# Performance work log

Measured on AMD Instinct MI355X. Metric: run time of the kernel, lower is better.

## Reference

```python
import jax, jax.numpy as jnp
import numpy as np

WIN = 3  # win_size from init


def setup_inputs() -> dict:
    key = jax.random.key(0)
    ks = jax.random.split(key, 7)
    B, H, W, d = 8, 128, 128, 128
    N = H * W
    s = d ** -0.5  # param init scale
    return {
        "x": jax.random.normal(ks[0], (B, N, d), dtype=jnp.float32),
        "Wq": jax.random.normal(ks[1], (d, d), dtype=jnp.float32) * s,
        "bq": jax.random.normal(ks[2], (d,), dtype=jnp.float32) * 0.01,
        "Wk": jax.random.normal(ks[3], (d, d), dtype=jnp.float32) * s,
        "bk": jax.random.normal(ks[4], (d,), dtype=jnp.float32) * 0.01,
        "Wv": jax.random.normal(ks[5], (d, d), dtype=jnp.float32) * s,
        "bv": jax.random.normal(ks[6], (d,), dtype=jnp.float32) * 0.01,
        "H": H,
        "W": W,
    }


def reference(x, Wq, bq, Wk, bk, Wv, bv, H, W):
    B, N, d = x.shape
    scale = d ** -0.5
    pad = WIN // 2

    q = (x @ Wq + bq).reshape(B, H, W, d)
    k = (x @ Wk + bk).reshape(B, H, W, d)
    v = (x @ Wv + bv).reshape(B, H, W, d)

    # zero-pad spatial dims (matches F.pad); padded neighbors get logit 0, not -inf
    k_pad = jnp.pad(k, ((0, 0), (pad, pad), (pad, pad), (0, 0)))
    v_pad = jnp.pad(v, ((0, 0), (pad, pad), (pad, pad), (0, 0)))

    scores_l, vs_l = [], []
    for dy in range(WIN):
        for dx in range(WIN):
            k_slice = k_pad[:, dy:dy + H, dx:dx + W]   # [B,H,W,d]
            v_slice = v_pad[:, dy:dy + H, dx:dx + W]
            scores_l.append(jnp.einsum("bhwd,bhwd->bhw", q, k_slice) * scale)
            vs_l.append(v_slice)

    scores = jnp.stack(scores_l, axis=-1)            # [B,H,W,9]
    prob = jax.nn.softmax(scores, axis=-1)           # [B,H,W,9]
    v_stk = jnp.stack(vs_l, axis=-1)                 # [B,H,W,d,9]
    out = jnp.einsum("bhwn,bhwdn->bhwd", prob, v_stk)
    return out.reshape(B, N, d)
```

## Files before the change

kernel.cpp:

```cpp
#include <hip/hip_runtime.h>
#include <stdint.h>

#define B_ 8
#define H_ 128
#define W_ 128
#define D_ 128
#define N_ (H_*W_)
#define M_ (B_*N_)

typedef __attribute__((ext_vector_type(8))) short short8;
typedef __attribute__((ext_vector_type(4))) float floatx4;

typedef const __attribute__((address_space(1))) void* gas_t;
typedef __attribute__((address_space(3))) void* las_t;

__device__ inline unsigned short f2bf(float f){
  union { float f; unsigned int i; } c; c.f = f;
  unsigned int x = c.i;
  x += 0x7FFF + ((x >> 16) & 1);
  return (unsigned short)(x >> 16);
}
__device__ inline float bflo(unsigned int u){
  union { unsigned int i; float f; } c; c.i = u << 16; return c.f;
}
__device__ inline float bfhi(unsigned int u){
  union { unsigned int i; float f; } c; c.i = u & 0xFFFF0000u; return c.f;
}

__global__ void wtrans_kernel(const float* __restrict__ Wq, const float* __restrict__ Wk,
                              const float* __restrict__ Wv, unsigned short* __restrict__ Wt){
  const float* src = blockIdx.x == 0 ? Wq : (blockIdx.x == 1 ? Wk : Wv);
  unsigned short* dst = Wt + blockIdx.x * (D_*D_);
  const int i = blockIdx.y * 256 + threadIdx.x;
  const int k = i >> 7, n = i & 127;
  dst[n*D_ + k] = f2bf(src[i]);
}

__global__ __launch_bounds__(256, 2) void qkv_gemm_kernel(
    const float* __restrict__ x, const unsigned short* __restrict__ Wt,
    const float* __restrict__ bq, const float* __restrict__ bk, const float* __restrict__ bv,
    unsigned short* __restrict__ Q, unsigned short* __restrict__ K, unsigned short* __restrict__ V)
{
  const int which = blockIdx.x;
  const int rowTile = blockIdx.y;
  const float* bias = which == 0 ? bq : (which == 1 ? bk : bv);
  unsigned short* Out = which == 0 ? Q : (which == 1 ? K : V);
  const unsigned short* Wsel = Wt + which * (D_*D_);

  __shared__ unsigned short lds[32768];

  const int t = threadIdx.x;
  const int wave = t >> 6, lane = t & 63;

  {
    #pragma unroll
    for (int p = 0; p < 8; ++p){
      int s = p*256 + t;
      int n = s >> 4, cp = s & 15, c = cp ^ (n & 7);
      const unsigned short* gp = Wsel + n*128 + c*8;
      unsigned short* lp = (unsigned short*)lds + 16384 + p*2048 + wave*512;
      __builtin_amdgcn_global_load_lds((gas_t)(const void*)gp, (las_t)(void*)lp, 16, 0, 0);
    }
  }
  {
    const float* xrow = x + (size_t)rowTile * 128 * D_;
    #pragma unroll
    for (int p = 0; p < 8; ++p){
      int s = p*256 + t;
      int r = s >> 4, cp = s & 15, c = cp ^ (r & 7);
      const float* gp = xrow + r*D_ + c*8;
      float4 f0 = *(const float4*)gp;
      float4 f1 = *(const float4*)(gp + 4);
      uint4 pk;
      pk.x = (unsigned)f2bf(f0.x) | ((unsigned)f2bf(f0.y) << 16);
      pk.y = (unsigned)f2bf(f0.z) | ((unsigned)f2bf(f0.w) << 16);
      pk.z = (unsigned)f2bf(f1.x) | ((unsigned)f2bf(f1.y) << 16);
      pk.w = (unsigned)f2bf(f1.z) | ((unsigned)f2bf(f1.w) << 16);
      *(uint4*)&lds[s*8] = pk;
    }
  }
  __syncthreads();

  const int wm = (wave >> 1) * 64, wn = (wave & 1) * 64;
  const int m0 = lane & 15, quad = lane >> 4;

  floatx4 acc[4][4] = {};
  #pragma unroll
  for (int kk = 0; kk < 4; ++kk){
    short8 a[4], b[4];
    #pragma unroll
    for (int i = 0; i < 4; ++i){
      int row = wm + i*16 + m0;
      int c = (kk*4 + quad) ^ (row & 7);
      a[i] = *(const short8*)&lds[row*128 + c*8];
    }
    #pragma unroll
    for (int j = 0; j < 4; ++j){
      int n = wn + j*16 + m0;
      int c = (kk*4 + quad) ^ (n & 7);
      b[j] = *(const short8*)&lds[16384 + n*128 + c*8];
    }
    #pragma unroll
    for (int i = 0; i < 4; ++i)
      #pragma unroll
      for (int j = 0; j < 4; ++j)
        acc[i][j] = __builtin_amdgcn_mfma_f32_16x16x32_bf16(a[i], b[j], acc[i][j], 0, 0, 0);
  }

  __syncthreads();
  #pragma unroll
  for (int j = 0; j < 4; ++j){
    const int col = wn + j*16 + m0;
    const float bb = bias[col];
    #pragma unroll
    for (int i = 0; i < 4; ++i){
      #pragma unroll
      for (int r = 0; r < 4; ++r){
        int row = wm + i*16 + quad*4 + r;
        lds[row*136 + col] = f2bf(acc[i][j][r] + bb);
      }
    }
  }
  __syncthreads();
  unsigned short* Outp = Out + (size_t)rowTile * 128 * D_;
  #pragma unroll
  for (int p = 0; p < 8; ++p){
    int rr = p*16 + (t >> 4), cc = t & 15;
    uint4 v = *(const uint4*)&lds[rr*136 + cc*8];
    *(uint4*)(Outp + p*2048 + t*8) = v;
  }
}

__global__ __launch_bounds__(256) void attn_kernel(
    const unsigned short* __restrict__ Q, const unsigned short* __restrict__ K,
    const unsigned short* __restrict__ V, float* __restrict__ out)
{
  const int t = threadIdx.x;
  const int quarter = t & 3;
  const int pix = blockIdx.x * 64 + (t >> 2);
  const int w = pix & 127;
  const int h = (pix >> 7) & 127;
  const float scale = 0.08838834764831845f;

  const size_t off = (size_t)pix * D_ + quarter * 32;

  float q[32];
  {
    const unsigned short* qp = Q + off;
    #pragma unroll
    for (int c = 0; c < 4; ++c){
      uint4 u = *(const uint4*)(qp + c*8);
      unsigned uu[4] = {u.x, u.y, u.z, u.w};
      #pragma unroll
      for (int e = 0; e < 4; ++e){
        q[c*8 + e*2]     = bflo(uu[e]) * scale;
        q[c*8 + e*2 + 1] = bfhi(uu[e]) * scale;
      }
    }
  }

  float s[9];
  #pragma unroll
  for (int i = 0; i < 9; ++i){
    const int dy = i/3 - 1, dx = i%3 - 1;
    const bool ok = ((unsigned)(h + dy) < 128u) && ((unsigned)(w + dx) < 128u);
    float acc = 0.f;
    if (ok){
      const unsigned short* kp = K + off + (dy*W_ + dx) * D_;
      #pragma unroll
      for (int c = 0; c < 4; ++c){
        uint4 u = *(const uint4*)(kp + c*8);
        unsigned uu[4] = {u.x, u.y, u.z, u.w};
        #pragma unroll
        for (int e = 0; e < 4; ++e){
          acc += q[c*8 + e*2]     * bflo(uu[e]);
          acc += q[c*8 + e*2 + 1] * bfhi(uu[e]);
        }
      }
    }
    s[i] = acc;
  }
  #pragma unroll
  for (int i = 0; i < 9; ++i){
    s[i] += __shfl_xor(s[i], 1, 64);
    s[i] += __shfl_xor(s[i], 2, 64);
  }

  float m = s[0];
  #pragma unroll
  for (int i = 1; i < 9; ++i) m = fmaxf(m, s[i]);
  float p[9]; float l = 0.f;
  #pragma unroll
  for (int i = 0; i < 9; ++i){ p[i] = __expf(s[i] - m); l += p[i]; }
  const float inv = 1.f / l;

  float o[32];
  #pragma unroll
  for (int d = 0; d < 32; ++d) o[d] = 0.f;
  #pragma unroll
  for (int i = 0; i < 9; ++i){
    const int dy = i/3 - 1, dx = i%3 - 1;
    const bool ok = ((unsigned)(h + dy) < 128u) && ((unsigned)(w + dx) < 128u);
    if (ok){
      const float pi = p[i];
      const unsigned short* vp = V + off + (dy*W_ + dx) * D_;
      #pragma unroll
      for (int c = 0; c < 4; ++c){
        uint4 u = *(const uint4*)(vp + c*8);
        unsigned uu[4] = {u.x, u.y, u.z, u.w};
        #pragma unroll
        for (int e = 0; e < 4; ++e){
          o[c*8 + e*2]     += pi * bflo(uu[e]);
          o[c*8 + e*2 + 1] += pi * bfhi(uu[e]);
        }
      }
    }
  }

  float* op = out + off;
  #pragma unroll
  for (int c = 0; c < 8; ++c){
    float4 v4 = make_float4(o[c*4]*inv, o[c*4+1]*inv, o[c*4+2]*inv, o[c*4+3]*inv);
    *(float4*)(op + c*4) = v4;
  }
}

extern "C" void kernel_launch(void* const* d_in, const int* in_sizes, int n_in,
                              void* d_out, int out_size, void* d_ws, size_t ws_size,
                              hipStream_t stream)
{
  const float* x  = (const float*)d_in[0];
  const float* Wq = (const float*)d_in[1];
  const float* bq = (const float*)d_in[2];
  const float* Wk = (const float*)d_in[3];
  const float* bk = (const float*)d_in[4];
  const float* Wv = (const float*)d_in[5];
  const float* bv = (const float*)d_in[6];
  float* out = (float*)d_out;

  char* ws = (char*)d_ws;
  unsigned short* Wt = (unsigned short*)ws;
  unsigned short* Q  = (unsigned short*)(ws + (1<<17));
  unsigned short* K  = (unsigned short*)(ws + (1<<17) + (size_t)M_*D_*2);
  unsigned short* V  = (unsigned short*)(ws + (1<<17) + (size_t)2*M_*D_*2);

  hipLaunchKernelGGL(wtrans_kernel, dim3(3, 64), dim3(256), 0, stream, Wq, Wk, Wv, Wt);
  hipLaunchKernelGGL(qkv_gemm_kernel, dim3(3, M_/128), dim3(256), 0, stream,
                     x, Wt, bq, bk, bv, Q, K, V);
  hipLaunchKernelGGL(attn_kernel, dim3(M_/64), dim3(256), 0, stream, Q, K, V, out);
}
```

Baseline: 220.7 us.

## Stage 10x10 K/V halo tiles in LDS for 8x8 pixel attention blocks

The attention kernel now gives each block an 8x8 spatial tile. It loads a zero-padded 10x10 halo of K into shared memory, computes the scores, then reuses the same buffer for V. This replaces nine global gathers per pixel with one cooperative load per tile, aiming to cut redundant L2/HBM traffic and the boundary branches. In exchange it adds two extra barriers, about 26KB of LDS per block (which limits occupancy), and halo overhead of roughly 1.56x. The 134-element padded row stride is meant to reduce bank conflicts.

Measured after the change: 278.0 us. 26.0% more time.

```diff
diff --git a/kernel.cpp b/kernel.cpp
--- a/kernel.cpp
+++ b/kernel.cpp
@@ -131,18 +131,41 @@
   }
 }
 
+#define SR_ 134
 __global__ __launch_bounds__(256) void attn_kernel(
     const unsigned short* __restrict__ Q, const unsigned short* __restrict__ K,
     const unsigned short* __restrict__ V, float* __restrict__ out)
 {
-  const int t = threadIdx.x;
+  __shared__ unsigned short sh[100 * SR_];
+
+  const int t  = threadIdx.x;
+  const int bx = blockIdx.x;
+  const int by = blockIdx.y;
+  const int bz = blockIdx.z;
+  const int gx0 = bx*8 - 1, gy0 = by*8 - 1;
+
+  #pragma unroll
+  for (int p = 0; p < 7; ++p){
+    int s = p*256 + t;
+    if (s < 1600){
+      int r = s >> 4, c = s & 15;
+      int ly = r / 10, lx = r - ly*10;
+      int py = gy0 + ly, px = gx0 + lx;
+      uint4 val = make_uint4(0,0,0,0);
+      if (((unsigned)py < 128u) && ((unsigned)px < 128u)){
+        size_t pix = ((size_t)bz*N_ + py*W_ + px);
+        val = *(const uint4*)(K + pix*D_ + c*8);
+      }
+      *(uint4*)&sh[r*SR_ + c*8] = val;
+    }
+  }
+
   const int quarter = t & 3;
-  const int pix = blockIdx.x * 64 + (t >> 2);
-  const int w = pix & 127;
-  const int h = (pix >> 7) & 127;
+  const int pi = t >> 2;
+  const int ty = pi >> 3, tx = pi & 7;
+  const size_t mypix = (size_t)bz*N_ + (by*8 + ty)*W_ + (bx*8 + tx);
+  const size_t off = mypix*D_ + quarter*32;
   const float scale = 0.08838834764831845f;
-
-  const size_t off = (size_t)pix * D_ + quarter * 32;
 
   float q[32];
   {
@@ -158,61 +181,76 @@
       }
     }
   }
-
-  float s[9];
+  __syncthreads();
+
+  float s9[9];
   #pragma unroll
   for (int i = 0; i < 9; ++i){
-    const int dy = i/3 - 1, dx = i%3 - 1;
-    const bool ok = ((unsigned)(h + dy) < 128u) && ((unsigned)(w + dx) < 128u);
+    const int dy = i/3, dx = i%3;
+    const int lr = (ty + dy)*10 + (tx + dx);
+    const unsigned short* kp = &sh[lr*SR_ + quarter*32];
     float acc = 0.f;
-    if (ok){
-      const unsigned short* kp = K + off + (dy*W_ + dx) * D_;
-      #pragma unroll
-      for (int c = 0; c < 4; ++c){
-        uint4 u = *(const uint4*)(kp + c*8);
-        unsigned uu[4] = {u.x, u.y, u.z, u.w};
-        #pragma unroll
-        for (int e = 0; e < 4; ++e){
-          acc += q[c*8 + e*2]     * bflo(uu[e]);
-          acc += q[c*8 + e*2 + 1] * bfhi(uu[e]);
-        }
-      }
-    }
-    s[i] = acc;
+    #pragma unroll
+    for (int c = 0; c < 4; ++c){
+      uint4 u = *(const uint4*)(kp + c*8);
+      unsigned uu[4] = {u.x, u.y, u.z, u.w};
+      #pragma unroll
+      for (int e = 0; e < 4; ++e){
+        acc += q[c*8 + e*2]     * bflo(uu[e]);
+        acc += q[c*8 + e*2 + 1] * bfhi(uu[e]);
+      }
+    }
+    s9[i] = acc;
   }
   #pragma unroll
   for (int i = 0; i < 9; ++i){
-    s[i] += __shfl_xor(s[i], 1, 64);
-    s[i] += __shfl_xor(s[i], 2, 64);
-  }
-
-  float m = s[0];
-  #pragma unroll
-  for (int i = 1; i < 9; ++i) m = fmaxf(m, s[i]);
-  float p[9]; float l = 0.f;
-  #pragma unroll
-  for (int i = 0; i < 9; ++i){ p[i] = __expf(s[i] - m); l += p[i]; }
+    s9[i] += __shfl_xor(s9[i], 1, 64);
+    s9[i] += __shfl_xor(s9[i], 2, 64);
+  }
+
+  float m = s9[0];
+  #pragma unroll
+  for (int i = 1; i < 9; ++i) m = fmaxf(m, s9[i]);
+  float p9[9]; float l = 0.f;
+  #pragma unroll
+  for (int i = 0; i < 9; ++i){ p9[i] = __expf(s9[i] - m); l += p9[i]; }
   const float inv = 1.f / l;
 
+  __syncthreads();
+  #pragma unroll
+  for (int p = 0; p < 7; ++p){
+    int s = p*256 + t;
+    if (s < 1600){
+      int r = s >> 4, c = s & 15;
+      int ly = r / 10, lx = r - ly*10;
+      int py = gy0 + ly, px = gx0 + lx;
+      uint4 val = make_uint4(0,0,0,0);
+      if (((unsigned)py < 128u) && ((unsigned)px < 128u)){
+        size_t pix = ((size_t)bz*N_ + py*W_ + px);
+        val = *(const uint4*)(V + pix*D_ + c*8);
+      }
+      *(uint4*)&sh[r*SR_ + c*8] = val;
+    }
+  }
+  __syncthreads();
+
   float o[32];
   #pragma unroll
   for (int d = 0; d < 32; ++d) o[d] = 0.f;
   #pragma unroll
   for (int i = 0; i < 9; ++i){
-    const int dy = i/3 - 1, dx = i%3 - 1;
-    const bool ok = ((unsigned)(h + dy) < 128u) && ((unsigned)(w + dx) < 128u);
-    if (ok){
-      const float pi = p[i];
-      const unsigned short* vp = V + off + (dy*W_ + dx) * D_;
-      #pragma unroll
-      for (int c = 0; c < 4; ++c){
-        uint4 u = *(const uint4*)(vp + c*8);
-        unsigned uu[4] = {u.x, u.y, u.z, u.w};
-        #pragma unroll
-        for (int e = 0; e < 4; ++e){
-          o[c*8 + e*2]     += pi * bflo(uu[e]);
-          o[c*8 + e*2 + 1] += pi * bfhi(uu[e]);
-        }
+    const int dy = i/3, dx = i%3;
+    const int lr = (ty + dy)*10 + (tx + dx);
+    const unsigned short* vp = &sh[lr*SR_ + quarter*32];
+    const float pi9 = p9[i];
+    #pragma unroll
+    for (int c = 0; c < 4; ++c){
+      uint4 u = *(const uint4*)(vp + c*8);
+      unsigned uu[4] = {u.x, u.y, u.z, u.w};
+      #pragma unroll
+      for (int e = 0; e < 4; ++e){
+        o[c*8 + e*2]     += pi9 * bflo(uu[e]);
+        o[c*8 + e*2 + 1] += pi9 * bfhi(uu[e]);
       }
     }
   }
@@ -247,5 +285,5 @@
   hipLaunchKernelGGL(wtrans_kernel, dim3(3, 64), dim3(256), 0, stream, Wq, Wk, Wv, Wt);
   hipLaunchKernelGGL(qkv_gemm_kernel, dim3(3, M_/128), dim3(256), 0, stream,
                      x, Wt, bq, bk, bv, Q, K, V);
-  hipLaunchKernelGGL(attn_kernel, dim3(M_/64), dim3(256), 0, stream, Q, K, V, out);
-}
+  hipLaunchKernelGGL(attn_kernel, dim3(16, 16, B_), dim3(256), 0, stream, Q, K, V, out);
+}
```
